# Optimization experiments

Measured on AMD Instinct MI355X. Metric: run time of the kernel, lower is better.

## Reference

```python
import jax, jax.numpy as jnp
import numpy as np

NHEADS = 16
LN_EPS = 1e-5


def setup_inputs() -> dict:
    key = jax.random.key(0)
    ks = jax.random.split(key, 12)
    B, L, D = 8, 1024, 1024
    bound = 1.0 / np.sqrt(D)
    inp = {
        'query': jax.random.normal(ks[0], (B, L, D), jnp.float32),
        'key':   jax.random.normal(ks[1], (B, L, D), jnp.float32),
        'value': jax.random.normal(ks[2], (B, L, D), jnp.float32),
        'q_mask': jnp.ones((B, L), jnp.float32),
        'k_mask': jnp.ones((B, L), jnp.float32),
        'Wq': jax.random.uniform(ks[3], (D, D), jnp.float32, -bound, bound),
        'bq': jax.random.uniform(ks[4], (D,), jnp.float32, -bound, bound),
        'Wk': jax.random.uniform(ks[5], (D, D), jnp.float32, -bound, bound),
        'bk': jax.random.uniform(ks[6], (D,), jnp.float32, -bound, bound),
        'Wv': jax.random.uniform(ks[7], (D, D), jnp.float32, -bound, bound),
        'bv': jax.random.uniform(ks[8], (D,), jnp.float32, -bound, bound),
        'Wo': jax.random.uniform(ks[9], (D, D), jnp.float32, -bound, bound),
        'bo': jax.random.uniform(ks[10], (D,), jnp.float32, -bound, bound),
        'gamma': jnp.ones((D,), jnp.float32),
        'beta': jnp.zeros((D,), jnp.float32),
    }
    return inp


def reference(query, key, value, q_mask, k_mask, Wq, bq, Wk, bk, Wv, bv, Wo, bo, gamma, beta):
    B, L, D = query.shape
    H = NHEADS
    d = D // H
    residual = query
    # linear projections (torch Linear: x @ W.T + b)
    q = query @ Wq.T + bq
    k = key @ Wk.T + bk
    v = value @ Wv.T + bv
    # NOTE: module does a raw contiguous view [B, L, H*d] -> [B*H, L, d]
    # (NOT a transpose-based head split). Replicate exactly.
    q = q.reshape(B * H, L, d)
    k = k.reshape(B * H, L, d)
    v = v.reshape(B * H, L, d)
    # masks tiled head-major: repeat(nheads, 1) -> [H*B, L]
    qm = jnp.tile(q_mask, (H, 1))
    km = jnp.tile(k_mask, (H, 1))
    mask = qm[:, :, None] * km[:, None, :]  # [B*H, L, L] outer product
    scores = jnp.einsum('bqd,bkd->bqk', q, k) / np.sqrt(d).astype(np.float32)
    A = jnp.exp(jnp.where(mask == 0, -jnp.inf, scores))  # unstable exp, as in source
    A_sum = jnp.clip(jnp.sum(A, axis=-1, keepdims=True), 2e-15, None)
    attn = A / A_sum
    context = (attn @ v).reshape(B, L, H * d)
    out = context @ Wo.T + bo
    # dropout is identity in eval mode
    x = residual + out
    mean = jnp.mean(x, axis=-1, keepdims=True)
    var = jnp.mean(jnp.square(x - mean), axis=-1, keepdims=True)
    return (x - mean) / jnp.sqrt(var + LN_EPS) * gamma + beta
```

## Files before the change

### kernel.cpp

```cpp
#include <hip/hip_runtime.h>
#include <hip/hip_bf16.h>


typedef __bf16 bf16x8 __attribute__((ext_vector_type(8)));
typedef float  f32x4  __attribute__((ext_vector_type(4)));

#define KK 1024
#define NN 1024

union BfPack4 { __bf16 h[4]; uint2 u; };
union BfPack8 { __bf16 h[8]; uint4 u; };

__device__ __forceinline__ void lds_copy16(void* lds, const void* gsrc) {
  __builtin_amdgcn_global_load_lds(
      (__attribute__((address_space(1))) void*)(uintptr_t)gsrc,
      (__attribute__((address_space(3))) void*)(unsigned int)(uintptr_t)lds,
      16, 0, 0);
}

struct Cvt4 { const float* src[4]; __bf16* dst; };

__global__ __launch_bounds__(256) void cvt_w(Cvt4 a) {
  const int z = blockIdx.y;
  const float* s = a.src[z];
  __bf16* d = a.dst + (size_t)z * (KK * NN);
  const int i = (blockIdx.x * 256 + threadIdx.x) * 4;
  float4 f = *(const float4*)&s[i];
  BfPack4 p;
  p.h[0] = (__bf16)f.x; p.h[1] = (__bf16)f.y;
  p.h[2] = (__bf16)f.z; p.h[3] = (__bf16)f.w;
  *(uint2*)&d[i] = p.u;
}

struct GQKV {
  const float*  A[3];
  const __bf16* W;
  const float*  bias[3];
  __bf16*       C[3];
};

__global__ __launch_bounds__(256) void gemm_qkv(GQKV args)
{
  __shared__ alignas(16) __bf16 As[128 * 40];
  __shared__ alignas(16) __bf16 Bs[128 * 32];
  const int z = blockIdx.z;
  const float*  A  = args.A[z];
  const __bf16* W  = args.W + (size_t)z * KK * NN;
  const float*  bias = args.bias[z];
  __bf16* C = args.C[z];
  const int tid = threadIdx.x, l = tid & 63, w = tid >> 6;
  const int m0 = blockIdx.x * 128, n0 = blockIdx.y * 128;
  const int lr = l & 15, lq = l >> 4;
  const int wm = (w & 1) * 64, wn = (w >> 1) * 64;

  const __bf16* gw0 = &W[(size_t)(n0 + (tid >> 2)) * KK + (tid & 3) * 8];
  const __bf16* gw1 = &W[(size_t)(n0 + 64 + (tid >> 2)) * KK + (tid & 3) * 8];
  char* lB0 = (char*)Bs + w * 1024;
  char* lB1 = (char*)Bs + 4096 + w * 1024;

  float4 pa[4];
  #pragma unroll
  for (int s = 0; s < 4; ++s) {
    int c = tid + 256 * s; int row = c >> 3, ko = (c & 7) * 4;
    pa[s] = *(const float4*)&A[(size_t)(m0 + row) * KK + ko];
  }

  f32x4 acc[4][4] = {};

  for (int kk = 0; kk < KK; kk += 32) {
    __syncthreads();
    #pragma unroll
    for (int s = 0; s < 4; ++s) {
      int c = tid + 256 * s; int row = c >> 3, ko = (c & 7) * 4;
      BfPack4 p;
      p.h[0] = (__bf16)pa[s].x; p.h[1] = (__bf16)pa[s].y;
      p.h[2] = (__bf16)pa[s].z; p.h[3] = (__bf16)pa[s].w;
      *(uint2*)&As[row * 40 + ko] = p.u;
    }
    lds_copy16(lB0, gw0 + kk);
    lds_copy16(lB1, gw1 + kk);
    __syncthreads();
    if (kk + 32 < KK) {
      #pragma unroll
      for (int s = 0; s < 4; ++s) {
        int c = tid + 256 * s; int row = c >> 3, ko = (c & 7) * 4;
        pa[s] = *(const float4*)&A[(size_t)(m0 + row) * KK + kk + 32 + ko];
      }
    }
    bf16x8 af[4], bf[4];
    #pragma unroll
    for (int t = 0; t < 4; ++t) {
      af[t] = *(const bf16x8*)&As[(wm + t * 16 + lr) * 40 + lq * 8];
      bf[t] = *(const bf16x8*)&Bs[(wn + t * 16 + lr) * 32 + lq * 8];
    }
    #pragma unroll
    for (int mt = 0; mt < 4; ++mt)
      #pragma unroll
      for (int nt = 0; nt < 4; ++nt)
        acc[mt][nt] = __builtin_amdgcn_mfma_f32_16x16x32_bf16(af[mt], bf[nt], acc[mt][nt], 0, 0, 0);
  }

  #pragma unroll
  for (int mt = 0; mt < 4; ++mt)
    #pragma unroll
    for (int nt = 0; nt < 4; ++nt)
      #pragma unroll
      for (int i = 0; i < 4; ++i) {
        int gm = m0 + wm + mt * 16 + lq * 4 + i;
        int gn = n0 + wn + nt * 16 + lr;
        C[(size_t)gm * NN + gn] = (__bf16)(acc[mt][nt][i] + bias[gn]);
      }
}

struct GO { const __bf16* A; const __bf16* W; const float* bias; float* C; };

__global__ __launch_bounds__(256) void gemm_out(GO args)
{
  __shared__ alignas(16) __bf16 As[128 * 32];
  __shared__ alignas(16) __bf16 Bs[128 * 32];
  const int tid = threadIdx.x, l = tid & 63, w = tid >> 6;
  const int m0 = blockIdx.x * 128, n0 = blockIdx.y * 128;
  const int lr = l & 15, lq = l >> 4;
  const int wm = (w & 1) * 64, wn = (w >> 1) * 64;

  const __bf16* ga0 = &args.A[(size_t)(m0 + (tid >> 2)) * KK + (tid & 3) * 8];
  const __bf16* ga1 = &args.A[(size_t)(m0 + 64 + (tid >> 2)) * KK + (tid & 3) * 8];
  const __bf16* gw0 = &args.W[(size_t)(n0 + (tid >> 2)) * KK + (tid & 3) * 8];
  const __bf16* gw1 = &args.W[(size_t)(n0 + 64 + (tid >> 2)) * KK + (tid & 3) * 8];
  char* lA0 = (char*)As + w * 1024;
  char* lA1 = (char*)As + 4096 + w * 1024;
  char* lB0 = (char*)Bs + w * 1024;
  char* lB1 = (char*)Bs + 4096 + w * 1024;

  f32x4 acc[4][4] = {};

  for (int kk = 0; kk < KK; kk += 32) {
    __syncthreads();
    lds_copy16(lA0, ga0 + kk);
    lds_copy16(lA1, ga1 + kk);
    lds_copy16(lB0, gw0 + kk);
    lds_copy16(lB1, gw1 + kk);
    __syncthreads();
    bf16x8 af[4], bf[4];
    #pragma unroll
    for (int t = 0; t < 4; ++t) {
      af[t] = *(const bf16x8*)&As[(wm + t * 16 + lr) * 32 + lq * 8];
      bf[t] = *(const bf16x8*)&Bs[(wn + t * 16 + lr) * 32 + lq * 8];
    }
    #pragma unroll
    for (int mt = 0; mt < 4; ++mt)
      #pragma unroll
      for (int nt = 0; nt < 4; ++nt)
        acc[mt][nt] = __builtin_amdgcn_mfma_f32_16x16x32_bf16(af[mt], bf[nt], acc[mt][nt], 0, 0, 0);
  }

  #pragma unroll
  for (int mt = 0; mt < 4; ++mt)
    #pragma unroll
    for (int nt = 0; nt < 4; ++nt)
      #pragma unroll
      for (int i = 0; i < 4; ++i) {
        int gm = m0 + wm + mt * 16 + lq * 4 + i;
        int gn = n0 + wn + nt * 16 + lr;
        args.C[(size_t)gm * NN + gn] = acc[mt][nt][i] + args.bias[gn];
      }
}

__global__ __launch_bounds__(256) void attn_kernel(
    const __bf16* __restrict__ qb, const __bf16* __restrict__ kb,
    const __bf16* __restrict__ vb, const float* __restrict__ qm,
    const float* __restrict__ km, __bf16* __restrict__ ctxb)
{
  const int g   = blockIdx.y;
  const int qt  = blockIdx.x;
  const int tid = threadIdx.x;
  const int l   = tid & 63;
  const int w   = tid >> 6;
  const int lr  = l & 15;
  const int lq  = l >> 4;

  __shared__ alignas(16) __bf16 Qs[64 * 72];
  __shared__ alignas(16) __bf16 Ks[128 * 72];
  __shared__ alignas(16) __bf16 Vt[64 * 136];
  __shared__ alignas(16) __bf16 Ps[64 * 136];

  const size_t gbase = (size_t)g * 1024 * 64;
  const __bf16* qg = qb + gbase;
  const __bf16* kg = kb + gbase;
  const __bf16* vg = vb + gbase;
  const float* qmrow = qm + (size_t)(g & 7) * 1024;
  const float* kmrow = km + (size_t)(g & 7) * 1024;

  #pragma unroll
  for (int s = 0; s < 2; ++s) {
    int ch = tid + 256 * s;
    int row = ch >> 3, co = (ch & 7) * 8;
    *(uint4*)&Qs[row * 72 + co] = *(const uint4*)&qg[(size_t)(qt * 64 + row) * 64 + co];
  }

  float qmv[4];
  #pragma unroll
  for (int i = 0; i < 4; ++i) qmv[i] = qmrow[qt * 64 + w * 16 + lq * 4 + i];

  __syncthreads();
  bf16x8 qa[2];
  qa[0] = *(const bf16x8*)&Qs[(w * 16 + lr) * 72 + lq * 8];
  qa[1] = *(const bf16x8*)&Qs[(w * 16 + lr) * 72 + 32 + lq * 8];

  float rs[4] = {};
  f32x4 ctx[4] = {};

  for (int kt = 0; kt < 8; ++kt) {
    __syncthreads();
    #pragma unroll
    for (int s = 0; s < 4; ++s) {
      int ch = tid + 256 * s;
      int row = ch >> 3, co = (ch & 7) * 8;
      *(uint4*)&Ks[row * 72 + co] = *(const uint4*)&kg[(size_t)(kt * 128 + row) * 64 + co];
    }
    #pragma unroll
    for (int s = 0; s < 4; ++s) {
      int ch = tid + 256 * s;
      int c0 = ch >> 7, j = ch & 127;
      BfPack8 vv;
      vv.u = *(const uint4*)&vg[(size_t)(kt * 128 + j) * 64 + c0 * 8];
      #pragma unroll
      for (int cc = 0; cc < 8; ++cc)
        Vt[(c0 * 8 + cc) * 136 + j] = vv.h[cc];
    }
    __syncthreads();

    f32x4 sacc[8];
    #pragma unroll
    for (int t = 0; t < 8; ++t) {
      bf16x8 kb0 = *(const bf16x8*)&Ks[(t * 16 + lr) * 72 + lq * 8];
      bf16x8 kb1 = *(const bf16x8*)&Ks[(t * 16 + lr) * 72 + 32 + lq * 8];
      f32x4 z = {};
      z = __builtin_amdgcn_mfma_f32_16x16x32_bf16(qa[0], kb0, z, 0, 0, 0);
      sacc[t] = __builtin_amdgcn_mfma_f32_16x16x32_bf16(qa[1], kb1, z, 0, 0, 0);
    }

    #pragma unroll
    for (int t = 0; t < 8; ++t) {
      float kmv = kmrow[kt * 128 + t * 16 + lr];
      #pragma unroll
      for (int i = 0; i < 4; ++i) {
        float e = (qmv[i] * kmv == 0.0f) ? 0.0f : __expf(sacc[t][i] * 0.125f);
        rs[i] += e;
        Ps[(w * 16 + lq * 4 + i) * 136 + t * 16 + lr] = (__bf16)e;
      }
    }

    #pragma unroll
    for (int ks = 0; ks < 4; ++ks) {
      bf16x8 pa = *(const bf16x8*)&Ps[(w * 16 + lr) * 136 + ks * 32 + lq * 8];
      #pragma unroll
      for (int ct = 0; ct < 4; ++ct) {
        bf16x8 vf = *(const bf16x8*)&Vt[(ct * 16 + lr) * 136 + ks * 32 + lq * 8];
        ctx[ct] = __builtin_amdgcn_mfma_f32_16x16x32_bf16(pa, vf, ctx[ct], 0, 0, 0);
      }
    }
  }

  #pragma unroll
  for (int i = 0; i < 4; ++i) {
    float v = rs[i];
    v += __shfl_xor(v, 1);
    v += __shfl_xor(v, 2);
    v += __shfl_xor(v, 4);
    v += __shfl_xor(v, 8);
    rs[i] = 1.0f / fmaxf(v, 2e-15f);
  }

  #pragma unroll
  for (int ct = 0; ct < 4; ++ct)
    #pragma unroll
    for (int i = 0; i < 4; ++i) {
      int row = w * 16 + lq * 4 + i;
      ctxb[gbase + (size_t)(qt * 64 + row) * 64 + ct * 16 + lr] =
          (__bf16)(ctx[ct][i] * rs[i]);
    }
}

__global__ __launch_bounds__(256) void ln_kernel(
    const float* __restrict__ O, const float* __restrict__ resid,
    const float* __restrict__ gam, const float* __restrict__ bet,
    float* __restrict__ out)
{
  const int row = blockIdx.x;
  const int tid = threadIdx.x;
  const float* orow = O + (size_t)row * 1024;
  const float* rrow = resid + (size_t)row * 1024;
  float x[4];
  float sum = 0.f, sq = 0.f;
  #pragma unroll
  for (int j = 0; j < 4; ++j) {
    int c = tid + j * 256;
    x[j] = orow[c] + rrow[c];
    sum += x[j];
    sq  += x[j] * x[j];
  }
  #pragma unroll
  for (int off = 32; off > 0; off >>= 1) {
    sum += __shfl_down(sum, off, 64);
    sq  += __shfl_down(sq, off, 64);
  }
  __shared__ float s1[4], s2[4];
  __shared__ float mean_s, inv_s;
  if ((tid & 63) == 0) { s1[tid >> 6] = sum; s2[tid >> 6] = sq; }
  __syncthreads();
  if (tid == 0) {
    float S = s1[0] + s1[1] + s1[2] + s1[3];
    float Q = s2[0] + s2[1] + s2[2] + s2[3];
    float mean = S * (1.0f / 1024.0f);
    float var  = fmaxf(Q * (1.0f / 1024.0f) - mean * mean, 0.0f);
    mean_s = mean;
    inv_s  = rsqrtf(var + 1e-5f);
  }
  __syncthreads();
  float mean = mean_s, inv = inv_s;
  #pragma unroll
  for (int j = 0; j < 4; ++j) {
    int c = tid + j * 256;
    out[(size_t)row * 1024 + c] = (x[j] - mean) * inv * gam[c] + bet[c];
  }
}

extern "C" void kernel_launch(void* const* d_in, const int* in_sizes, int n_in,
                              void* d_out, int out_size, void* d_ws, size_t ws_size,
                              hipStream_t stream)
{
  const float* query = (const float*)d_in[0];
  const float* keyi  = (const float*)d_in[1];
  const float* value = (const float*)d_in[2];
  const float* qmask = (const float*)d_in[3];
  const float* kmask = (const float*)d_in[4];
  const float* Wq = (const float*)d_in[5];
  const float* bq = (const float*)d_in[6];
  const float* Wk = (const float*)d_in[7];
  const float* bk = (const float*)d_in[8];
  const float* Wv = (const float*)d_in[9];
  const float* bv = (const float*)d_in[10];
  const float* Wo = (const float*)d_in[11];
  const float* bo = (const float*)d_in[12];
  const float* gam = (const float*)d_in[13];
  const float* bet = (const float*)d_in[14];

  char* ws = (char*)d_ws;
  __bf16* qbuf = (__bf16*)(ws);
  __bf16* kbuf = (__bf16*)(ws + ((size_t)16 << 20));
  __bf16* vbuf = (__bf16*)(ws + ((size_t)32 << 20));
  __bf16* wb   = (__bf16*)(ws + ((size_t)48 << 20));
  float*  obuf = (float*)(ws + ((size_t)16 << 20));

  Cvt4 cv;
  cv.src[0] = Wq; cv.src[1] = Wk; cv.src[2] = Wv; cv.src[3] = Wo;
  cv.dst = wb;

  GQKV qkv;
  qkv.A[0] = query; qkv.A[1] = keyi; qkv.A[2] = value;
  qkv.W = wb;
  qkv.bias[0] = bq; qkv.bias[1] = bk; qkv.bias[2] = bv;
  qkv.C[0] = qbuf;  qkv.C[1] = kbuf; qkv.C[2] = vbuf;

  GO op;
  op.A = qbuf;
  op.W = wb + (size_t)3 * KK * NN;
  op.bias = bo;
  op.C = obuf;

  dim3 tb(256);
  hipLaunchKernelGGL(cvt_w, dim3(1024, 4), tb, 0, stream, cv);
  hipLaunchKernelGGL(gemm_qkv, dim3(64, 8, 3), tb, 0, stream, qkv);
  hipLaunchKernelGGL(attn_kernel, dim3(16, 128), tb, 0, stream, qbuf, kbuf, vbuf, qmask, kmask, qbuf);
  hipLaunchKernelGGL(gemm_out, dim3(64, 8), tb, 0, stream, op);
  hipLaunchKernelGGL(ln_kernel, dim3(8192), tb, 0, stream, obuf, query, gam, bet, (float*)d_out);
}
```

Measured before the change: 402.9 us.

## Double-buffer GEMM tiles and restructure attention with async loads and larger query tiles

Both projection GEMMs now double-buffer their LDS weight/activation tiles: the next K-slice is issued via global_load_lds while MFMAs run on the current one. gemm_out also drops one barrier per iteration. The attention kernel now processes 128 query rows per block, with each wave doing two row tiles. It loads Q/K with asynchronous global-to-LDS copies, prefetches the next V tile into registers, and stages the key mask in LDS as bf16. P is stored in a swizzled, narrower buffer processed in two halves. These changes target memory latency and global-load overhead, at the cost of more LDS, more registers and half as many attention blocks.

```diff
diff --git a/kernel.cpp b/kernel.cpp
--- a/kernel.cpp
+++ b/kernel.cpp
@@ -42,10 +42,10 @@
 __global__ __launch_bounds__(256) void gemm_qkv(GQKV args)
 {
   __shared__ alignas(16) __bf16 As[128 * 40];
-  __shared__ alignas(16) __bf16 Bs[128 * 32];
+  __shared__ alignas(16) __bf16 Bs[2][4096];
   const int z = blockIdx.z;
-  const float*  A  = args.A[z];
-  const __bf16* W  = args.W + (size_t)z * KK * NN;
+  const float*  A    = args.A[z];
+  const __bf16* W    = args.W + (size_t)z * KK * NN;
   const float*  bias = args.bias[z];
   __bf16* C = args.C[z];
   const int tid = threadIdx.x, l = tid & 63, w = tid >> 6;
@@ -55,8 +55,6 @@
 
   const __bf16* gw0 = &W[(size_t)(n0 + (tid >> 2)) * KK + (tid & 3) * 8];
   const __bf16* gw1 = &W[(size_t)(n0 + 64 + (tid >> 2)) * KK + (tid & 3) * 8];
-  char* lB0 = (char*)Bs + w * 1024;
-  char* lB1 = (char*)Bs + 4096 + w * 1024;
 
   float4 pa[4];
   #pragma unroll
@@ -64,9 +62,11 @@
     int c = tid + 256 * s; int row = c >> 3, ko = (c & 7) * 4;
     pa[s] = *(const float4*)&A[(size_t)(m0 + row) * KK + ko];
   }
+  lds_copy16((char*)Bs + w * 1024,        gw0);
+  lds_copy16((char*)Bs + 4096 + w * 1024, gw1);
 
   f32x4 acc[4][4] = {};
-
+  int ib = 0;
   for (int kk = 0; kk < KK; kk += 32) {
     __syncthreads();
     #pragma unroll
@@ -77,27 +77,29 @@
       p.h[2] = (__bf16)pa[s].z; p.h[3] = (__bf16)pa[s].w;
       *(uint2*)&As[row * 40 + ko] = p.u;
     }
-    lds_copy16(lB0, gw0 + kk);
-    lds_copy16(lB1, gw1 + kk);
     __syncthreads();
     if (kk + 32 < KK) {
+      lds_copy16((char*)Bs + (ib ^ 1) * 8192 + w * 1024,        gw0 + kk + 32);
+      lds_copy16((char*)Bs + (ib ^ 1) * 8192 + 4096 + w * 1024, gw1 + kk + 32);
       #pragma unroll
       for (int s = 0; s < 4; ++s) {
         int c = tid + 256 * s; int row = c >> 3, ko = (c & 7) * 4;
         pa[s] = *(const float4*)&A[(size_t)(m0 + row) * KK + kk + 32 + ko];
       }
     }
+    const __bf16* Bb = (const __bf16*)((char*)Bs + ib * 8192);
     bf16x8 af[4], bf[4];
     #pragma unroll
     for (int t = 0; t < 4; ++t) {
       af[t] = *(const bf16x8*)&As[(wm + t * 16 + lr) * 40 + lq * 8];
-      bf[t] = *(const bf16x8*)&Bs[(wn + t * 16 + lr) * 32 + lq * 8];
+      bf[t] = *(const bf16x8*)&Bb[(wn + t * 16 + lr) * 32 + lq * 8];
     }
     #pragma unroll
     for (int mt = 0; mt < 4; ++mt)
       #pragma unroll
       for (int nt = 0; nt < 4; ++nt)
         acc[mt][nt] = __builtin_amdgcn_mfma_f32_16x16x32_bf16(af[mt], bf[nt], acc[mt][nt], 0, 0, 0);
+    ib ^= 1;
   }
 
   #pragma unroll
@@ -116,8 +118,8 @@
 
 __global__ __launch_bounds__(256) void gemm_out(GO args)
 {
-  __shared__ alignas(16) __bf16 As[128 * 32];
-  __shared__ alignas(16) __bf16 Bs[128 * 32];
+  __shared__ alignas(16) __bf16 As[2][4096];
+  __shared__ alignas(16) __bf16 Bs[2][4096];
   const int tid = threadIdx.x, l = tid & 63, w = tid >> 6;
   const int m0 = blockIdx.x * 128, n0 = blockIdx.y * 128;
   const int lr = l & 15, lq = l >> 4;
@@ -127,31 +129,36 @@
   const __bf16* ga1 = &args.A[(size_t)(m0 + 64 + (tid >> 2)) * KK + (tid & 3) * 8];
   const __bf16* gw0 = &args.W[(size_t)(n0 + (tid >> 2)) * KK + (tid & 3) * 8];
   const __bf16* gw1 = &args.W[(size_t)(n0 + 64 + (tid >> 2)) * KK + (tid & 3) * 8];
-  char* lA0 = (char*)As + w * 1024;
-  char* lA1 = (char*)As + 4096 + w * 1024;
-  char* lB0 = (char*)Bs + w * 1024;
-  char* lB1 = (char*)Bs + 4096 + w * 1024;
+
+  lds_copy16((char*)As + w * 1024,        ga0);
+  lds_copy16((char*)As + 4096 + w * 1024, ga1);
+  lds_copy16((char*)Bs + w * 1024,        gw0);
+  lds_copy16((char*)Bs + 4096 + w * 1024, gw1);
 
   f32x4 acc[4][4] = {};
-
+  int ib = 0;
   for (int kk = 0; kk < KK; kk += 32) {
     __syncthreads();
-    lds_copy16(lA0, ga0 + kk);
-    lds_copy16(lA1, ga1 + kk);
-    lds_copy16(lB0, gw0 + kk);
-    lds_copy16(lB1, gw1 + kk);
-    __syncthreads();
+    if (kk + 32 < KK) {
+      lds_copy16((char*)As + (ib ^ 1) * 8192 + w * 1024,        ga0 + kk + 32);
+      lds_copy16((char*)As + (ib ^ 1) * 8192 + 4096 + w * 1024, ga1 + kk + 32);
+      lds_copy16((char*)Bs + (ib ^ 1) * 8192 + w * 1024,        gw0 + kk + 32);
+      lds_copy16((char*)Bs + (ib ^ 1) * 8192 + 4096 + w * 1024, gw1 + kk + 32);
+    }
+    const __bf16* Ab = (const __bf16*)((char*)As + ib * 8192);
+    const __bf16* Bb = (const __bf16*)((char*)Bs + ib * 8192);
     bf16x8 af[4], bf[4];
     #pragma unroll
     for (int t = 0; t < 4; ++t) {
-      af[t] = *(const bf16x8*)&As[(wm + t * 16 + lr) * 32 + lq * 8];
-      bf[t] = *(const bf16x8*)&Bs[(wn + t * 16 + lr) * 32 + lq * 8];
+      af[t] = *(const bf16x8*)&Ab[(wm + t * 16 + lr) * 32 + lq * 8];
+      bf[t] = *(const bf16x8*)&Bb[(wn + t * 16 + lr) * 32 + lq * 8];
     }
     #pragma unroll
     for (int mt = 0; mt < 4; ++mt)
       #pragma unroll
       for (int nt = 0; nt < 4; ++nt)
         acc[mt][nt] = __builtin_amdgcn_mfma_f32_16x16x32_bf16(af[mt], bf[nt], acc[mt][nt], 0, 0, 0);
+    ib ^= 1;
   }
 
   #pragma unroll
@@ -171,20 +178,17 @@
     const __bf16* __restrict__ vb, const float* __restrict__ qm,
     const float* __restrict__ km, __bf16* __restrict__ ctxb)
 {
-  const int g   = blockIdx.y;
-  const int qt  = blockIdx.x;
-  const int tid = threadIdx.x;
-  const int l   = tid & 63;
-  const int w   = tid >> 6;
-  const int lr  = l & 15;
-  const int lq  = l >> 4;
-
-  __shared__ alignas(16) __bf16 Qs[64 * 72];
-  __shared__ alignas(16) __bf16 Ks[128 * 72];
+  const int g  = blockIdx.y;
+  const int qt = blockIdx.x;
+  const int tid = threadIdx.x, l = tid & 63, w = tid >> 6;
+  const int lr = l & 15, lq = l >> 4;
+
+  __shared__ alignas(16) __bf16 Ps[128 * 72];
+  __shared__ alignas(16) __bf16 Ks[2 * 128 * 32];
   __shared__ alignas(16) __bf16 Vt[64 * 136];
-  __shared__ alignas(16) __bf16 Ps[64 * 136];
-
-  const size_t gbase = (size_t)g * 1024 * 64;
+  __shared__ alignas(16) __bf16 kms[1024];
+
+  const size_t gbase = (size_t)g * (1024 * 64);
   const __bf16* qg = qb + gbase;
   const __bf16* kg = kb + gbase;
   const __bf16* vg = vb + gbase;
@@ -192,94 +196,146 @@
   const float* kmrow = km + (size_t)(g & 7) * 1024;
 
   #pragma unroll
-  for (int s = 0; s < 2; ++s) {
-    int ch = tid + 256 * s;
-    int row = ch >> 3, co = (ch & 7) * 8;
-    *(uint4*)&Qs[row * 72 + co] = *(const uint4*)&qg[(size_t)(qt * 64 + row) * 64 + co];
-  }
-
-  float qmv[4];
-  #pragma unroll
-  for (int i = 0; i < 4; ++i) qmv[i] = qmrow[qt * 64 + w * 16 + lq * 4 + i];
+  for (int s = 0; s < 4; ++s) {
+    int c = tid + 256 * s;
+    int p = c >> 9, r = (c >> 2) & 127, q0 = c & 3;
+    lds_copy16((char*)Ps + w * 1024 + s * 4096,
+               &qg[(size_t)(qt * 128 + r) * 64 + p * 32 + q0 * 8]);
+  }
+  {
+    float4 kf = *(const float4*)&kmrow[tid * 4];
+    BfPack4 p;
+    p.h[0] = (__bf16)(kf.x == 0.f ? 0.f : 1.f);
+    p.h[1] = (__bf16)(kf.y == 0.f ? 0.f : 1.f);
+    p.h[2] = (__bf16)(kf.z == 0.f ? 0.f : 1.f);
+    p.h[3] = (__bf16)(kf.w == 0.f ? 0.f : 1.f);
+    *(uint2*)&kms[tid * 4] = p.u;
+  }
+  float qmv[2][4];
+  #pragma unroll
+  for (int rt = 0; rt < 2; ++rt)
+    #pragma unroll
+    for (int i = 0; i < 4; ++i)
+      qmv[rt][i] = qmrow[qt * 128 + 32 * w + rt * 16 + lq * 4 + i];
 
   __syncthreads();
-  bf16x8 qa[2];
-  qa[0] = *(const bf16x8*)&Qs[(w * 16 + lr) * 72 + lq * 8];
-  qa[1] = *(const bf16x8*)&Qs[(w * 16 + lr) * 72 + 32 + lq * 8];
-
-  float rs[4] = {};
-  f32x4 ctx[4] = {};
+
+  bf16x8 qa[2][2];
+  #pragma unroll
+  for (int rt = 0; rt < 2; ++rt)
+    #pragma unroll
+    for (int p = 0; p < 2; ++p)
+      qa[rt][p] = *(const bf16x8*)((char*)Ps + p * 8192 +
+                                   (32 * w + rt * 16 + lr) * 64 + lq * 16);
+
+  uint4 pv[4];
+  #pragma unroll
+  for (int s = 0; s < 4; ++s) {
+    int ch = tid + 256 * s; int j = ch & 127, c0 = ch >> 7;
+    pv[s] = *(const uint4*)&vg[(size_t)j * 64 + c0 * 8];
+  }
+
+  float rs[2][4] = {};
+  f32x4 ctx[2][4] = {};
 
   for (int kt = 0; kt < 8; ++kt) {
     __syncthreads();
     #pragma unroll
     for (int s = 0; s < 4; ++s) {
-      int ch = tid + 256 * s;
-      int row = ch >> 3, co = (ch & 7) * 8;
-      *(uint4*)&Ks[row * 72 + co] = *(const uint4*)&kg[(size_t)(kt * 128 + row) * 64 + co];
+      int c = tid + 256 * s;
+      int p = c >> 9, r = (c >> 2) & 127, q0 = c & 3;
+      lds_copy16((char*)Ks + w * 1024 + s * 4096,
+                 &kg[(size_t)(kt * 128 + r) * 64 + p * 32 + q0 * 8]);
     }
     #pragma unroll
     for (int s = 0; s < 4; ++s) {
-      int ch = tid + 256 * s;
-      int c0 = ch >> 7, j = ch & 127;
-      BfPack8 vv;
-      vv.u = *(const uint4*)&vg[(size_t)(kt * 128 + j) * 64 + c0 * 8];
+      int ch = tid + 256 * s; int j = ch & 127, c0 = ch >> 7;
+      BfPack8 vv; vv.u = pv[s];
       #pragma unroll
       for (int cc = 0; cc < 8; ++cc)
         Vt[(c0 * 8 + cc) * 136 + j] = vv.h[cc];
     }
     __syncthreads();
-
-    f32x4 sacc[8];
-    #pragma unroll
-    for (int t = 0; t < 8; ++t) {
-      bf16x8 kb0 = *(const bf16x8*)&Ks[(t * 16 + lr) * 72 + lq * 8];
-      bf16x8 kb1 = *(const bf16x8*)&Ks[(t * 16 + lr) * 72 + 32 + lq * 8];
-      f32x4 z = {};
-      z = __builtin_amdgcn_mfma_f32_16x16x32_bf16(qa[0], kb0, z, 0, 0, 0);
-      sacc[t] = __builtin_amdgcn_mfma_f32_16x16x32_bf16(qa[1], kb1, z, 0, 0, 0);
-    }
-
-    #pragma unroll
-    for (int t = 0; t < 8; ++t) {
-      float kmv = kmrow[kt * 128 + t * 16 + lr];
+    if (kt < 7) {
+      #pragma unroll
+      for (int s = 0; s < 4; ++s) {
+        int ch = tid + 256 * s; int j = ch & 127, c0 = ch >> 7;
+        pv[s] = *(const uint4*)&vg[(size_t)((kt + 1) * 128 + j) * 64 + c0 * 8];
+      }
+    }
+    const int wkey = 16 * (lq >> 1);
+    const int rkey = 16 * ((lr >> 3) & 1);
+    #pragma unroll
+    for (int h = 0; h < 2; ++h) {
+      f32x4 sacc[2][4];
+      #pragma unroll
+      for (int c4 = 0; c4 < 4; ++c4) {
+        int ct = h * 4 + c4;
+        bf16x8 kb0 = *(const bf16x8*)((char*)Ks + (ct * 16 + lr) * 64 + lq * 16);
+        bf16x8 kb1 = *(const bf16x8*)((char*)Ks + 8192 + (ct * 16 + lr) * 64 + lq * 16);
+        #pragma unroll
+        for (int rt = 0; rt < 2; ++rt) {
+          f32x4 zz = {};
+          zz = __builtin_amdgcn_mfma_f32_16x16x32_bf16(qa[rt][0], kb0, zz, 0, 0, 0);
+          sacc[rt][c4] = __builtin_amdgcn_mfma_f32_16x16x32_bf16(qa[rt][1], kb1, zz, 0, 0, 0);
+        }
+      }
+      #pragma unroll
+      for (int c4 = 0; c4 < 4; ++c4) {
+        int ct = h * 4 + c4;
+        float kmv = (float)kms[kt * 128 + ct * 16 + lr];
+        #pragma unroll
+        for (int rt = 0; rt < 2; ++rt)
+          #pragma unroll
+          for (int i = 0; i < 4; ++i) {
+            float e = (qmv[rt][i] * kmv == 0.f) ? 0.f
+                                                : __expf(sacc[rt][c4][i] * 0.125f);
+            rs[rt][i] += e;
+            int row = 32 * w + rt * 16 + lq * 4 + i;
+            Ps[row * 72 + ((c4 * 16 + lr) ^ wkey)] = (__bf16)e;
+          }
+      }
+      #pragma unroll
+      for (int ks = 0; ks < 2; ++ks) {
+        bf16x8 pa[2];
+        #pragma unroll
+        for (int rt = 0; rt < 2; ++rt)
+          pa[rt] = *(const bf16x8*)&Ps[(32 * w + rt * 16 + lr) * 72 +
+                                       ((ks * 32 + lq * 8) ^ rkey)];
+        #pragma unroll
+        for (int c2 = 0; c2 < 4; ++c2) {
+          bf16x8 vf = *(const bf16x8*)&Vt[(c2 * 16 + lr) * 136 +
+                                          h * 64 + ks * 32 + lq * 8];
+          #pragma unroll
+          for (int rt = 0; rt < 2; ++rt)
+            ctx[rt][c2] = __builtin_amdgcn_mfma_f32_16x16x32_bf16(pa[rt], vf, ctx[rt][c2], 0, 0, 0);
+        }
+      }
+    }
+  }
+
+  #pragma unroll
+  for (int rt = 0; rt < 2; ++rt)
+    #pragma unroll
+    for (int i = 0; i < 4; ++i) {
+      float v = rs[rt][i];
+      v += __shfl_xor(v, 1);
+      v += __shfl_xor(v, 2);
+      v += __shfl_xor(v, 4);
+      v += __shfl_xor(v, 8);
+      rs[rt][i] = 1.0f / fmaxf(v, 2e-15f);
+    }
+
+  #pragma unroll
+  for (int rt = 0; rt < 2; ++rt)
+    #pragma unroll
+    for (int c2 = 0; c2 < 4; ++c2)
       #pragma unroll
       for (int i = 0; i < 4; ++i) {
-        float e = (qmv[i] * kmv == 0.0f) ? 0.0f : __expf(sacc[t][i] * 0.125f);
-        rs[i] += e;
-        Ps[(w * 16 + lq * 4 + i) * 136 + t * 16 + lr] = (__bf16)e;
-      }
-    }
-
-    #pragma unroll
-    for (int ks = 0; ks < 4; ++ks) {
-      bf16x8 pa = *(const bf16x8*)&Ps[(w * 16 + lr) * 136 + ks * 32 + lq * 8];
-      #pragma unroll
-      for (int ct = 0; ct < 4; ++ct) {
-        bf16x8 vf = *(const bf16x8*)&Vt[(ct * 16 + lr) * 136 + ks * 32 + lq * 8];
-        ctx[ct] = __builtin_amdgcn_mfma_f32_16x16x32_bf16(pa, vf, ctx[ct], 0, 0, 0);
-      }
-    }
-  }
-
-  #pragma unroll
-  for (int i = 0; i < 4; ++i) {
-    float v = rs[i];
-    v += __shfl_xor(v, 1);
-    v += __shfl_xor(v, 2);
-    v += __shfl_xor(v, 4);
-    v += __shfl_xor(v, 8);
-    rs[i] = 1.0f / fmaxf(v, 2e-15f);
-  }
-
-  #pragma unroll
-  for (int ct = 0; ct < 4; ++ct)
-    #pragma unroll
-    for (int i = 0; i < 4; ++i) {
-      int row = w * 16 + lq * 4 + i;
-      ctxb[gbase + (size_t)(qt * 64 + row) * 64 + ct * 16 + lr] =
-          (__bf16)(ctx[ct][i] * rs[i]);
-    }
+        int row = qt * 128 + 32 * w + rt * 16 + lq * 4 + i;
+        ctxb[gbase + (size_t)row * 64 + c2 * 16 + lr] =
+            (__bf16)(ctx[rt][c2][i] * rs[rt][i]);
+      }
 }
 
 __global__ __launch_bounds__(256) void ln_kernel(
@@ -372,7 +428,7 @@
   dim3 tb(256);
   hipLaunchKernelGGL(cvt_w, dim3(1024, 4), tb, 0, stream, cv);
   hipLaunchKernelGGL(gemm_qkv, dim3(64, 8, 3), tb, 0, stream, qkv);
-  hipLaunchKernelGGL(attn_kernel, dim3(16, 128), tb, 0, stream, qbuf, kbuf, vbuf, qmask, kmask, qbuf);
+  hipLaunchKernelGGL(attn_kernel, dim3(8, 128), tb, 0, stream, qbuf, kbuf, vbuf, qmask, kmask, qbuf);
   hipLaunchKernelGGL(gemm_out, dim3(64, 8), tb, 0, stream, op);
   hipLaunchKernelGGL(ln_kernel, dim3(8192), tb, 0, stream, obuf, query, gam, bet, (float*)d_out);
 }
```

After: 402.4 us. About the same (-0.1%).
